# Optimization experiments

Hardware: AMD Instinct MI355X
Metric: run time of the kernel (lower is better)

## Reference

```python
import jax
import jax.numpy as jnp
import numpy as np
from jax import lax

# Butterworth order-2 lowpass, Wn=0.25 (scipy.signal.butter(2, 0.25))
_B = [0.0976310729378175, 0.195262145875635, 0.0976310729378175]
_A = [1.0, -0.9428090415820634, 0.33333333333333337]


def setup_inputs() -> dict:
    key = jax.random.key(0)
    x = jax.random.normal(key, (128, 8, 32768), dtype=jnp.float32)
    b = jnp.array(_B, dtype=jnp.float32)
    a = jnp.array(_A, dtype=jnp.float32)
    return {"x": x, "b": b, "a": a}


def _odd_ext(x, n):
    # scipy-style odd extension along the last axis
    left = 2.0 * x[..., :1] - x[..., 1:n + 1][..., ::-1]
    right = 2.0 * x[..., -1:] - x[..., -n - 1:-1][..., ::-1]
    return jnp.concatenate([left, x, right], axis=-1)


def _lfilter(b, a, x):
    # Direct-form II transposed IIR filter along last axis, zero initial state.
    b = b / a[0]
    a = a / a[0]
    order = b.shape[0] - 1  # static
    b_tail, a_tail = b[1:], a[1:]
    z0 = jnp.zeros(x.shape[:-1] + (order,), dtype=x.dtype)
    xT = jnp.moveaxis(x, -1, 0)  # [T, ...batch]

    def step(z, xt):
        yt = b[0] * xt + z[..., 0]
        z_shift = jnp.concatenate([z[..., 1:], jnp.zeros_like(z[..., :1])], axis=-1)
        z_new = z_shift + b_tail * xt[..., None] - a_tail * yt[..., None]
        return z_new, yt

    _, yT = lax.scan(step, z0, xT)
    return jnp.moveaxis(yT, 0, -1)


def _filtfilt(x, a, b):
    y = _lfilter(b, a, x)
    y = _lfilter(b, a, y[..., ::-1])
    return y[..., ::-1]


def reference(x, b, a):
    scale = jnp.max(jnp.abs(x), axis=-1, keepdims=True)
    xn = x / scale
    padlen = 3 * max(int(a.shape[0]), int(b.shape[0]))  # static = 9
    xe = _odd_ext(xn, padlen)
    y = _filtfilt(xe, a, b)
    y = y[..., padlen:-padlen]
    return y * scale
```

## Files before the change

kernel.cpp:

```cpp
#include <hip/hip_runtime.h>


#define N_COLS 32768
#define PAD 9
#define LTOT  (N_COLS + 2 * PAD)
#define WF 16
#define WB 16
#define C  16
#define LANES 64
#define P   (C * LANES)
#define NSEG (N_COLS / P)
#define WIN (WF + C + WB)
#define SLICE (WF + P + WB)
#define NV4 (SLICE / 4)
#define WPB 4
#define TPB 256

#define SWZ(s) ((s) ^ ((((s) >> 4) & 7) << 2))

#define LDS_PHASE_FENCE() do { asm volatile("" ::: "memory"); \
                               __builtin_amdgcn_sched_barrier(0); } while (0)

__launch_bounds__(TPB, 8)
__global__ void filtfilt_kernel(const float* __restrict__ x,
                                const float* __restrict__ bco,
                                const float* __restrict__ aco,
                                float* __restrict__ out,
                                int rows) {
    __shared__ __align__(128) float xs_all[WPB][SLICE];
    const int tid = threadIdx.x;
    const int wid = tid >> 6;
    const int lane = tid & 63;
    float* __restrict__ xs = xs_all[wid];

    const int W = blockIdx.x * WPB + wid;
    const int row = W >> 5;
    const int seg = W & (NSEG - 1);
    if (row >= rows) return;

    const float inv_a0 = 1.0f / aco[0];
    const float B0 = bco[0] * inv_a0;
    const float B1 = bco[1] * inv_a0;
    const float B2 = bco[2] * inv_a0;
    const float A1 = aco[1] * inv_a0;
    const float A2 = aco[2] * inv_a0;

    const float* __restrict__ xrow = x + (size_t)row * N_COLS;
    const int xoff = seg * P - WF;

#pragma unroll
    for (int m = 0; m < 5; ++m) {
        int i = lane + LANES * m;
        i = (i > NV4 - 1) ? (NV4 - 1) : i;
        int g = xoff + 4 * i;
        g = (g < 0) ? 0 : g;
        g = (g > N_COLS - 4) ? (N_COLS - 4) : g;
        *(float4*)(xs + SWZ(4 * i)) = *(const float4*)(xrow + g);
    }
    LDS_PHASE_FENCE();

    if (seg == 0 && lane < WF) {
        const int t = lane - (WF - PAD);
        xs[SWZ(lane)] = (t < 0) ? 0.0f : (2.0f * xrow[0] - xrow[PAD - t]);
    }
    if (seg == NSEG - 1 && lane < WF) {
        const int s = SLICE - WF + lane;
        xs[SWZ(s)] = (lane < PAD)
                   ? (2.0f * xrow[N_COLS - 1] - xrow[N_COLS - 2 - lane])
                   : 0.0f;
    }
    LDS_PHASE_FENCE();

    const int s0 = C * lane;
    float v[WIN];
#pragma unroll
    for (int j = 0; j < WIN / 4; ++j)
        *(float4*)(v + 4 * j) = *(const float4*)(xs + SWZ(s0 + 4 * j));
    {
        float z0 = 0.0f, z1 = 0.0f;
#pragma unroll
        for (int k = 0; k < WIN; ++k) {
            const float xv = v[k];
            const float y = fmaf(B0, xv, z0);
            z0 = fmaf(-A1, y, fmaf(B1, xv, z1));
            z1 = fmaf(B2, xv, -A2 * y);
            if (k >= WF) v[k] = y;
        }
    }
    if (seg == NSEG - 1 && lane == LANES - 1) {
#pragma unroll
        for (int k = 41; k < WIN; ++k) v[k] = 0.0f;
    }
    {
        float z0 = 0.0f, z1 = 0.0f;
#pragma unroll
        for (int k = WIN - 1; k >= WF; --k) {
            const float xv = v[k];
            const float y = fmaf(B0, xv, z0);
            z0 = fmaf(-A1, y, fmaf(B1, xv, z1));
            z1 = fmaf(B2, xv, -A2 * y);
            if (k < WF + C) v[k] = y;
        }
    }
    LDS_PHASE_FENCE();

#pragma unroll
    for (int j = 0; j < C / 4; ++j)
        *(float4*)(xs + SWZ(s0 + WF + 4 * j)) = *(const float4*)(v + WF + 4 * j);
    LDS_PHASE_FENCE();

    float* __restrict__ orow = out + (size_t)row * N_COLS + seg * P;
#pragma unroll
    for (int m = 0; m < P / 4 / LANES; ++m) {
        const int i = lane + LANES * m;
        *(float4*)(orow + 4 * i) = *(const float4*)(xs + SWZ(WF + 4 * i));
    }
}

extern "C" void kernel_launch(void* const* d_in, const int* in_sizes, int n_in,
                              void* d_out, int out_size, void* d_ws, size_t ws_size,
                              hipStream_t stream) {
    const float* x = (const float*)d_in[0];
    const float* b = (const float*)d_in[1];
    const float* a = (const float*)d_in[2];
    float* out = (float*)d_out;
    const int rows = out_size / N_COLS;
    const int total_waves = rows * NSEG;
    const int blocks = total_waves / WPB;
    filtfilt_kernel<<<blocks, TPB, 0, stream>>>(x, b, a, out, rows);
}
```

Baseline: 231.8 us.

## Make each wave loop over eight segments with register prefetch of next slice

Each wave now processes eight consecutive segments of a row instead of one. The global loads for the next segment are issued into registers before the current segment's filtering runs, so memory latency overlaps with compute. The grid shrinks by a factor of eight and launch bounds drop to four blocks per CU. The aim is to hide load latency and amortize per-wave setup, at the cost of more registers and less occupancy.

```diff
diff --git a/kernel.cpp b/kernel.cpp
--- a/kernel.cpp
+++ b/kernel.cpp
@@ -13,6 +13,7 @@
 #define WIN (WF + C + WB)
 #define SLICE (WF + P + WB)
 #define NV4 (SLICE / 4)
+#define NITER 8
 #define WPB 4
 #define TPB 256
 
@@ -21,7 +22,7 @@
 #define LDS_PHASE_FENCE() do { asm volatile("" ::: "memory"); \
                                __builtin_amdgcn_sched_barrier(0); } while (0)
 
-__launch_bounds__(TPB, 8)
+__launch_bounds__(TPB, 4)
 __global__ void filtfilt_kernel(const float* __restrict__ x,
                                 const float* __restrict__ bco,
                                 const float* __restrict__ aco,
@@ -33,9 +34,9 @@
     const int lane = tid & 63;
     float* __restrict__ xs = xs_all[wid];
 
-    const int W = blockIdx.x * WPB + wid;
-    const int row = W >> 5;
-    const int seg = W & (NSEG - 1);
+    const int g = blockIdx.x * WPB + wid;
+    const int row = g >> 2;
+    const int segbase = (g & 3) * NITER;
     if (row >= rows) return;
 
     const float inv_a0 = 1.0f / aco[0];
@@ -46,74 +47,99 @@
     const float A2 = aco[2] * inv_a0;
 
     const float* __restrict__ xrow = x + (size_t)row * N_COLS;
-    const int xoff = seg * P - WF;
+    float* __restrict__ orow0 = out + (size_t)row * N_COLS;
+
+    float4 pf[5];
+    auto issue = [&](int xoff) {
+#pragma unroll
+        for (int m = 0; m < 4; ++m) {
+            int gg = xoff + 4 * (lane + LANES * m);
+            gg = (gg < 0) ? 0 : gg;
+            gg = (gg > N_COLS - 4) ? (N_COLS - 4) : gg;
+            pf[m] = *(const float4*)(xrow + gg);
+        }
+        {
+            int gg = xoff + 4 * (256 + (lane & 7));
+            gg = (gg < 0) ? 0 : gg;
+            gg = (gg > N_COLS - 4) ? (N_COLS - 4) : gg;
+            pf[4] = *(const float4*)(xrow + gg);
+        }
+    };
+
+    issue(segbase * P - WF);
+
+    for (int it = 0; it < NITER; ++it) {
+        const int seg = segbase + it;
+        const int xoff = seg * P - WF;
 
 #pragma unroll
-    for (int m = 0; m < 5; ++m) {
-        int i = lane + LANES * m;
-        i = (i > NV4 - 1) ? (NV4 - 1) : i;
-        int g = xoff + 4 * i;
-        g = (g < 0) ? 0 : g;
-        g = (g > N_COLS - 4) ? (N_COLS - 4) : g;
-        *(float4*)(xs + SWZ(4 * i)) = *(const float4*)(xrow + g);
-    }
-    LDS_PHASE_FENCE();
+        for (int m = 0; m < 4; ++m)
+            *(float4*)(xs + SWZ(4 * (lane + LANES * m))) = pf[m];
+        if (lane < 8)
+            *(float4*)(xs + SWZ(4 * (256 + lane))) = pf[4];
+        LDS_PHASE_FENCE();
 
-    if (seg == 0 && lane < WF) {
-        const int t = lane - (WF - PAD);
-        xs[SWZ(lane)] = (t < 0) ? 0.0f : (2.0f * xrow[0] - xrow[PAD - t]);
-    }
-    if (seg == NSEG - 1 && lane < WF) {
-        const int s = SLICE - WF + lane;
-        xs[SWZ(s)] = (lane < PAD)
-                   ? (2.0f * xrow[N_COLS - 1] - xrow[N_COLS - 2 - lane])
-                   : 0.0f;
-    }
-    LDS_PHASE_FENCE();
+        if (seg == 0 && lane < WF) {
+            const int t = lane - (WF - PAD);
+            xs[SWZ(lane)] = (t < 0) ? 0.0f
+                                    : (2.0f * xrow[0] - xrow[PAD - t]);
+        }
+        if (seg == NSEG - 1 && lane < WF) {
+            const int s = SLICE - WF + lane;
+            xs[SWZ(s)] = (lane < PAD)
+                       ? (2.0f * xrow[N_COLS - 1] - xrow[N_COLS - 2 - lane])
+                       : 0.0f;
+        }
+        LDS_PHASE_FENCE();
 
-    const int s0 = C * lane;
-    float v[WIN];
+        if (it < NITER - 1) issue(xoff + P);
+
+        const int s0 = C * lane;
+        float v[WIN];
 #pragma unroll
-    for (int j = 0; j < WIN / 4; ++j)
-        *(float4*)(v + 4 * j) = *(const float4*)(xs + SWZ(s0 + 4 * j));
-    {
-        float z0 = 0.0f, z1 = 0.0f;
+        for (int j = 0; j < WIN / 4; ++j)
+            *(float4*)(v + 4 * j) = *(const float4*)(xs + SWZ(s0 + 4 * j));
+
+        {
+            float z0 = 0.0f, z1 = 0.0f;
 #pragma unroll
-        for (int k = 0; k < WIN; ++k) {
-            const float xv = v[k];
-            const float y = fmaf(B0, xv, z0);
-            z0 = fmaf(-A1, y, fmaf(B1, xv, z1));
-            z1 = fmaf(B2, xv, -A2 * y);
-            if (k >= WF) v[k] = y;
+            for (int k = 0; k < WIN; ++k) {
+                const float xv = v[k];
+                const float y = fmaf(B0, xv, z0);
+                z0 = fmaf(-A1, y, fmaf(B1, xv, z1));
+                z1 = fmaf(B2, xv, -A2 * y);
+                if (k >= WF) v[k] = y;
+            }
         }
-    }
-    if (seg == NSEG - 1 && lane == LANES - 1) {
+        if (seg == NSEG - 1 && lane == LANES - 1) {
 #pragma unroll
-        for (int k = 41; k < WIN; ++k) v[k] = 0.0f;
-    }
-    {
-        float z0 = 0.0f, z1 = 0.0f;
+            for (int k = 41; k < WIN; ++k) v[k] = 0.0f;
+        }
+        {
+            float z0 = 0.0f, z1 = 0.0f;
 #pragma unroll
-        for (int k = WIN - 1; k >= WF; --k) {
-            const float xv = v[k];
-            const float y = fmaf(B0, xv, z0);
-            z0 = fmaf(-A1, y, fmaf(B1, xv, z1));
-            z1 = fmaf(B2, xv, -A2 * y);
-            if (k < WF + C) v[k] = y;
+            for (int k = WIN - 1; k >= WF; --k) {
+                const float xv = v[k];
+                const float y = fmaf(B0, xv, z0);
+                z0 = fmaf(-A1, y, fmaf(B1, xv, z1));
+                z1 = fmaf(B2, xv, -A2 * y);
+                if (k < WF + C) v[k] = y;
+            }
         }
-    }
-    LDS_PHASE_FENCE();
+        LDS_PHASE_FENCE();
 
 #pragma unroll
-    for (int j = 0; j < C / 4; ++j)
-        *(float4*)(xs + SWZ(s0 + WF + 4 * j)) = *(const float4*)(v + WF + 4 * j);
-    LDS_PHASE_FENCE();
+        for (int j = 0; j < C / 4; ++j)
+            *(float4*)(xs + SWZ(s0 + WF + 4 * j)) = *(const float4*)(v + WF + 4 * j);
+        LDS_PHASE_FENCE();
 
-    float* __restrict__ orow = out + (size_t)row * N_COLS + seg * P;
+        float* __restrict__ orow = orow0 + seg * P;
 #pragma unroll
-    for (int m = 0; m < P / 4 / LANES; ++m) {
-        const int i = lane + LANES * m;
-        *(float4*)(orow + 4 * i) = *(const float4*)(xs + SWZ(WF + 4 * i));
+        for (int m = 0; m < 4; ++m) {
+            const int i = lane + LANES * m;
+            *(float4*)(orow + 4 * i) = *(const float4*)(xs + SWZ(WF + 4 * i));
+        }
+        LDS_PHASE_FENCE();
     }
 }
 
@@ -125,7 +151,7 @@
     const float* a = (const float*)d_in[2];
     float* out = (float*)d_out;
     const int rows = out_size / N_COLS;
-    const int total_waves = rows * NSEG;
-    const int blocks = total_waves / WPB;
+    const int total_waves = rows * (NSEG / NITER);
+    const int blocks = (total_waves + WPB - 1) / WPB;
     filtfilt_kernel<<<blocks, TPB, 0, stream>>>(x, b, a, out, rows);
 }
```

After: 258.8 us. +11.7%, slower.
